# Performance work log

Hardware: AMD Instinct MI355X
Metric: run time of the kernel (lower is better)

Reference implementation:

```python
import jax, jax.numpy as jnp
import numpy as np

N = 100000
E = 1_600_000
D_IN, D_HID, D_OUT = 100, 512, 200
NUM_PATH_AGG = 5   # walks per node in sample_neighbors_and_aggregate
MAX_LEN = 4        # max walk length (incl. start node)
NUM_PATH_FINAL = 10  # global paths in sample_path


def _build_nbr(src, dst, n):
    """Padded neighbor table [n, max_deg] (int32) + degree vector [n]."""
    deg = np.zeros(n, np.int64)
    np.add.at(deg, src, 1)
    maxd = max(int(deg.max()), 1)
    nbr = np.zeros((n, maxd), np.int32)
    order = np.argsort(src, kind='stable')
    ssrc, sdst = src[order], dst[order]
    offs = np.zeros(n + 1, np.int64)
    offs[1:] = np.cumsum(deg)
    rank = np.arange(len(ssrc)) - offs[ssrc]
    nbr[ssrc, rank] = sdst
    return jnp.asarray(nbr), jnp.asarray(deg.astype(np.int32))


def setup_inputs() -> dict:
    key = jax.random.key(0)
    ks = jax.random.split(key, 4)
    x = jax.random.normal(ks[0], (N, D_IN), jnp.float32)
    edge_index = jax.random.randint(ks[1], (2, E), 0, N, jnp.int64)
    ei = np.asarray(edge_index)
    src, dst = ei[0], ei[1]
    # directed neighbor list (get_neighbor_list)
    nbr_dir, deg_dir = _build_nbr(src, dst, N)
    # bi-directional neighbor list (reverse edge added unless self-loop)
    m = src != dst
    nbr_bi, deg_bi = _build_nbr(np.concatenate([src, dst[m]]),
                                np.concatenate([dst, src[m]]), N)
    W1 = jax.random.normal(ks[2], (D_HID, D_IN), jnp.float32) * 0.05
    b1 = jnp.zeros((D_HID,), jnp.float32)
    W3 = jax.random.normal(ks[3], (D_OUT, D_HID), jnp.float32) * 0.05
    b3 = jnp.zeros((D_OUT,), jnp.float32)
    return dict(x=x, edge_index=edge_index, nbr_bi=nbr_bi, deg_bi=deg_bi,
                nbr_dir=nbr_dir, deg_dir=deg_dir, W1=W1, b1=b1, W3=W3, b3=b3)


def _random_walk(key, starts, nbr, deg, extra_steps):
    """Vectorized random walks. Returns nodes [L, M], masks [L, M] (bool).
    A step is invalid (walk stopped) once the current node has no neighbors."""
    cur = starts
    valid = jnp.ones(starts.shape, bool)
    nodes, masks = [cur], [valid]
    for j in range(extra_steps):
        u = jax.random.uniform(jax.random.fold_in(key, j), starts.shape)
        d = deg[cur]
        choice = jnp.minimum((u * d.astype(u.dtype)).astype(jnp.int32),
                             jnp.maximum(d - 1, 0))
        valid = valid & (d > 0)
        cur = jnp.where(valid, nbr[cur, choice], cur)
        nodes.append(cur)
        masks.append(valid)
    return jnp.stack(nodes), jnp.stack(masks)


def reference(x, edge_index, nbr_bi, deg_bi, nbr_dir, deg_dir, W1, b1, W3, b3):
    n = x.shape[0]
    kw = jax.random.key(42)
    # out = relu(fc1(x))
    h = jax.nn.relu(x @ W1.T + b1)  # [N, D_HID]

    # sample_neighbors_and_aggregate: 5 walks of length<=4 starting at every node
    starts1 = jnp.tile(jnp.arange(n, dtype=jnp.int32), NUM_PATH_AGG)  # [5N]
    nodes1, masks1 = _random_walk(jax.random.fold_in(kw, 0), starts1,
                                  nbr_bi, deg_bi, MAX_LEN - 1)
    # [L, 5N] -> [L*5, N]; tile concatenates copies so axis split is (L, 5, N)
    entries = nodes1.reshape(MAX_LEN, NUM_PATH_AGG, n).reshape(-1, n)
    mentries = masks1.reshape(MAX_LEN, NUM_PATH_AGG, n).reshape(-1, n)

    def body(carry, sm):
        acc, cnt = carry
        s, m = sm
        acc = acc + jnp.where(m[:, None], h[s], 0.0)  # masked gather [N, D_HID]
        cnt = cnt + m.astype(h.dtype)
        return (acc, cnt), None

    (acc, cnt), _ = jax.lax.scan(
        body, (jnp.zeros_like(h), jnp.zeros((n,), h.dtype)), (entries, mentries))
    agg = acc / cnt[:, None]  # per-node mean over visited nodes (cnt >= 5)

    # out = relu(fc3(agg))
    out2 = jax.nn.relu(agg @ W3.T + b3)  # [N, D_OUT]

    # sample_path: 10 walks from random start nodes on the DIRECTED graph
    starts2 = jax.random.randint(jax.random.fold_in(kw, 1),
                                 (NUM_PATH_FINAL,), 0, n, jnp.int32)
    nodes2, masks2 = _random_walk(jax.random.fold_in(kw, 2), starts2,
                                  nbr_dir, deg_dir, MAX_LEN - 1)
    g = out2[nodes2]                         # [L, 10, D_OUT]
    w = masks2.astype(out2.dtype)            # [L, 10]
    mean = (g * w[..., None]).sum((0, 1)) / w.sum()
    return mean[None, None, :]               # [1, 1, D_OUT] (matches torch keepdims)
```

## Files before the change

### kernel.cpp

```cpp
#include <hip/hip_runtime.h>
#include <stdint.h>
#include <string.h>

#define JAX_THREEFRY_PARTITIONABLE 1

#define DIN 100
#define DHID 512
#define DOUT 200
#define NPATH_AGG 5
#define NFINAL 10
#define MAXLEN 4
#define NSLOT (MAXLEN * NFINAL)
#define NE 16
#define QSPLIT 8
#define NBLK_P1 (NSLOT * QSPLIT)

struct RngConsts {
  uint32_t kA[3][2];
  int      starts2[NFINAL];
  float    u2[3][NFINAL];
  int      N, maxd_bi, maxd_dir;
};

__host__ __device__ inline void tf2x32(uint32_t k0, uint32_t k1,
                                       uint32_t& x0, uint32_t& x1) {
  const uint32_t k2 = k0 ^ k1 ^ 0x1BD11BDAu;
  x0 += k0; x1 += k1;
#define TFR(r) { x0 += x1; x1 = (x1 << (r)) | (x1 >> (32 - (r))); x1 ^= x0; }
  TFR(13) TFR(15) TFR(26) TFR(6)
  x0 += k1; x1 += k2 + 1u;
  TFR(17) TFR(29) TFR(16) TFR(24)
  x0 += k2; x1 += k0 + 2u;
  TFR(13) TFR(15) TFR(26) TFR(6)
  x0 += k0; x1 += k1 + 3u;
  TFR(17) TFR(29) TFR(16) TFR(24)
  x0 += k1; x1 += k2 + 4u;
  TFR(13) TFR(15) TFR(26) TFR(6)
  x0 += k2; x1 += k0 + 5u;
#undef TFR
}

__host__ __device__ inline uint32_t jax_bits32(uint32_t k0, uint32_t k1,
                                               uint32_t idx, uint32_t half) {
#if JAX_THREEFRY_PARTITIONABLE
  (void)half;
  uint32_t x0 = 0u, x1 = idx;
  tf2x32(k0, k1, x0, x1);
  return x0 ^ x1;
#else
  uint32_t x0, x1;
  const bool lo = idx < half;
  if (lo) { x0 = idx;        x1 = idx + half; }
  else    { x0 = idx - half; x1 = idx;        }
  tf2x32(k0, k1, x0, x1);
  return lo ? x0 : x1;
#endif
}

__host__ __device__ inline float bits_to_unif(uint32_t bits) {
  uint32_t f = (bits >> 9) | 0x3F800000u;
  float r;
  memcpy(&r, &f, 4);
  return r - 1.0f;
}

__device__ __forceinline__ void walk_step(const int* __restrict__ nbr,
                                          const int* __restrict__ deg,
                                          int maxd, int lane, float u,
                                          int& cur, int& valid) {
  const int d = deg[cur];
  const long long base = (long long)cur * maxd;
  int r0 = 0, r1 = 0, r2 = 0, r3 = 0;
  if (lane < maxd)       r0 = nbr[base + lane];
  if (lane + 64 < maxd)  r1 = nbr[base + lane + 64];
  if (lane + 128 < maxd) r2 = nbr[base + lane + 128];
  if (lane + 192 < maxd) r3 = nbr[base + lane + 192];
  int c = (int)(u * (float)d);
  const int cm = (d - 1 > 0) ? (d - 1) : 0;
  if (c > cm) c = cm;
  const int cl = c & 63;
  const int v0 = __shfl(r0, cl);
  const int v1 = __shfl(r1, cl);
  const int v2 = __shfl(r2, cl);
  const int v3 = __shfl(r3, cl);
  int v = (c < 64) ? v0 : (c < 128) ? v1 : (c < 192) ? v2 : v3;
  if (c >= 256) v = nbr[base + c];
  valid = valid && (d > 0);
  if (valid) cur = v;
}

__device__ __forceinline__ void stage_row(const float* __restrict__ x,
                                          float* __restrict__ dst,
                                          int node, int lane) {
  if (lane < DIN / 2) {
    *(float2*)(dst + lane * 2) =
        *(const float2*)(x + (long long)node * DIN + lane * 2);
  }
}

__global__ __launch_bounds__(512) void k_slot(
    const float* __restrict__ x,
    const int* __restrict__ nbr_bi, const int* __restrict__ deg_bi,
    const int* __restrict__ nbr_dir, const int* __restrict__ deg_dir,
    const float* __restrict__ W1, const float* __restrict__ b1,
    RngConsts rc, int* __restrict__ maskArr, float* __restrict__ aggAll) {
  __shared__ int   vmask[NE];
  __shared__ float xs[NE][DIN];

  const int bid = blockIdx.x;
  const int tid = threadIdx.x;
  const int wv = tid >> 6, lane = tid & 63;
  const int slot = bid >> 3, q = bid & (QSPLIT - 1);
  const int w = slot % NFINAL, j = slot / NFINAL;

  int cur = rc.starts2[w];
  int valid = 1;
  for (int t = 0; t < j; ++t)
    walk_step(nbr_dir, deg_dir, rc.maxd_dir, lane, rc.u2[t][w], cur, valid);

  if (q == 0 && tid == 0) maskArr[slot] = valid;
  if (!valid) return;

  const int n = cur;
  if (tid == 0) vmask[0] = 1;

  if (wv < NPATH_AGG) {
    const uint32_t wkr = (uint32_t)(wv * rc.N + n);
    int c2 = n, v2 = 1;
#pragma unroll
    for (int jj = 0; jj < MAXLEN - 1; ++jj) {
      const float u = bits_to_unif(
          jax_bits32(rc.kA[jj][0], rc.kA[jj][1], wkr, 250000u));
      walk_step(nbr_bi, deg_bi, rc.maxd_bi, lane, u, c2, v2);
      const int ent = 1 + jj * NPATH_AGG + wv;
      if (lane == 0) vmask[ent] = v2;
      stage_row(x, &xs[ent][0], c2, lane);
    }
  } else if (wv == 5) {
    stage_row(x, &xs[0][0], n, lane);
  }
  __syncthreads();

  const int usub = tid >> 3, ks = tid & 7;
  const int unit = q * 64 + usub;
  const float4* __restrict__ w1r = (const float4*)(W1 + (long long)unit * DIN);
  float acc[NE];
#pragma unroll
  for (int e = 0; e < NE; ++e) acc[e] = 0.0f;
  for (int k4 = ks; k4 < DIN / 4; k4 += 8) {
    const float4 wv4 = w1r[k4];
#pragma unroll
    for (int e = 0; e < NE; ++e) {
      const float4 xv = *(const float4*)(&xs[e][k4 * 4]);
      acc[e] += wv4.x * xv.x + wv4.y * xv.y + wv4.z * xv.z + wv4.w * xv.w;
    }
  }
#pragma unroll
  for (int e = 0; e < NE; ++e) {
    float p = acc[e];
    p += __shfl_xor(p, 1);
    p += __shfl_xor(p, 2);
    p += __shfl_xor(p, 4);
    acc[e] = p;
  }
  if (ks == 0) {
    float cntf = 5.0f;
#pragma unroll
    for (int e = 1; e < NE; ++e) cntf += (float)vmask[e];
    const float bb = b1[unit];
    float h0 = acc[0] + bb;
    h0 = (h0 > 0.0f) ? h0 : 0.0f;
    float hs = 5.0f * h0;
#pragma unroll
    for (int e = 1; e < NE; ++e) {
      if (vmask[e]) {
        const float hv = acc[e] + bb;
        hs += (hv > 0.0f) ? hv : 0.0f;
      }
    }
    aggAll[(long long)slot * DHID + unit] = hs / cntf;
  }
}

__global__ __launch_bounds__(512) void k_fc3(
    const float* __restrict__ W3, const float* __restrict__ b3,
    const int* __restrict__ maskArr, const float* __restrict__ aggAll,
    float* __restrict__ out) {
  __shared__ int   maskS[NSLOT];
  __shared__ float partial[8];

  const int o = blockIdx.x;
  const int tid = threadIdx.x;
  const int wv = tid >> 6, lane = tid & 63;

  if (tid < NSLOT) maskS[tid] = maskArr[tid];
  __syncthreads();

  const float4* __restrict__ w4 = (const float4*)(W3 + (long long)o * DHID);
  const float4 g0 = w4[lane];
  const float4 g1 = w4[64 + lane];
  const float b3o = b3[o];

  float acc = 0.0f;
#pragma unroll
  for (int i = 0; i < NSLOT / 8; ++i) {
    const int s = wv + i * 8;
    if (maskS[s]) {
      const float4* a4 = (const float4*)(aggAll + (long long)s * DHID);
      const float4 a0 = a4[lane];
      const float4 a1 = a4[64 + lane];
      float p = a0.x * g0.x + a0.y * g0.y + a0.z * g0.z + a0.w * g0.w
              + a1.x * g1.x + a1.y * g1.y + a1.z * g1.z + a1.w * g1.w;
#pragma unroll
      for (int off = 32; off; off >>= 1) p += __shfl_xor(p, off);
      const float r = p + b3o;
      acc += (r > 0.0f) ? r : 0.0f;
    }
  }
  if (lane == 0) partial[wv] = acc;
  __syncthreads();
  if (tid == 0) {
    float wsum = 0.0f;
    for (int s = 0; s < NSLOT; ++s) wsum += (float)maskS[s];
    float tot = 0.0f;
#pragma unroll
    for (int v = 0; v < 8; ++v) tot += partial[v];
    out[o] = tot / wsum;
  }
}

static void h_enc(const uint32_t k[2], uint32_t x0, uint32_t x1, uint32_t out[2]) {
  tf2x32(k[0], k[1], x0, x1);
  out[0] = x0; out[1] = x1;
}
static void h_foldin(const uint32_t k[2], uint32_t data, uint32_t out[2]) {
  h_enc(k, 0u, data, out);
}

extern "C" void kernel_launch(void* const* d_in, const int* in_sizes, int n_in,
                              void* d_out, int out_size, void* d_ws, size_t ws_size,
                              hipStream_t stream) {
  const float* x       = (const float*)d_in[0];
  const int*   nbr_bi  = (const int*)d_in[2];
  const int*   deg_bi  = (const int*)d_in[3];
  const int*   nbr_dir = (const int*)d_in[4];
  const int*   deg_dir = (const int*)d_in[5];
  const float* W1      = (const float*)d_in[6];
  const float* b1      = (const float*)d_in[7];
  const float* W3      = (const float*)d_in[8];
  const float* b3      = (const float*)d_in[9];

  const int N = in_sizes[0] / DIN;
  RngConsts rc;
  rc.N = N;
  rc.maxd_bi  = in_sizes[2] / N;
  rc.maxd_dir = in_sizes[4] / N;

  const uint32_t kw[2] = {0u, 42u};
  uint32_t kA[2];
  h_foldin(kw, 0u, kA);
  for (uint32_t j = 0; j < 3; ++j) h_foldin(kA, j, rc.kA[j]);

  uint32_t kS[2];
  h_foldin(kw, 1u, kS);
  uint32_t k1_[2], k2_[2];
#if JAX_THREEFRY_PARTITIONABLE
  h_enc(kS, 0u, 0u, k1_);
  h_enc(kS, 0u, 1u, k2_);
#else
  {
    uint32_t a[2], b[2];
    h_enc(kS, 0u, 2u, a);
    h_enc(kS, 1u, 3u, b);
    k1_[0] = a[0]; k1_[1] = b[0];
    k2_[0] = a[1]; k2_[1] = b[1];
  }
#endif
  {
    const uint32_t span = (uint32_t)N;
    uint32_t mult = 65536u % span;
    mult = (uint32_t)(mult * mult) % span;
    for (uint32_t i = 0; i < NFINAL; ++i) {
      const uint32_t hi = jax_bits32(k1_[0], k1_[1], i, NFINAL / 2);
      const uint32_t lo = jax_bits32(k2_[0], k2_[1], i, NFINAL / 2);
      uint32_t off = (hi % span) * mult + (lo % span);
      off %= span;
      rc.starts2[i] = (int)off;
    }
  }

  uint32_t kP[2];
  h_foldin(kw, 2u, kP);
  for (uint32_t j = 0; j < 3; ++j) {
    uint32_t kPj[2];
    h_foldin(kP, j, kPj);
    for (uint32_t i = 0; i < NFINAL; ++i)
      rc.u2[j][i] = bits_to_unif(jax_bits32(kPj[0], kPj[1], i, NFINAL / 2));
  }

  int*   maskArr = (int*)d_ws;
  float* aggAll  = (float*)(maskArr + NSLOT);

  k_slot<<<NBLK_P1, 512, 0, stream>>>(x, nbr_bi, deg_bi, nbr_dir, deg_dir,
                                      W1, b1, rc, maskArr, aggAll);
  k_fc3<<<DOUT, 512, 0, stream>>>(W3, b3, maskArr, aggAll, (float*)d_out);
}
```

Baseline: 19.80 us.

## Fuse slot and fc3 kernels via atomic counter with last-arriving blocks computing fc3

Merges the two launches into one kernel. Each block bumps a global atomic counter after its slot work. The last 50 blocks to arrive each take 4 output units: they preload W3 rows, spin until all 320 blocks have finished, then do the fc3/ReLU/mean reduction. This removes the second kernel launch and its launch gap, at the cost of an extra memset, a spin-wait on the slowest block, and reliance on all blocks being co-resident or finishing in order.

```diff
diff --git a/kernel.cpp b/kernel.cpp
--- a/kernel.cpp
+++ b/kernel.cpp
@@ -14,6 +14,8 @@
 #define NE 16
 #define QSPLIT 8
 #define NBLK_P1 (NSLOT * QSPLIT)
+#define NSPIN 50
+#define OPB 4
 
 struct RngConsts {
   uint32_t kA[3][2];
@@ -98,14 +100,19 @@
   }
 }
 
-__global__ __launch_bounds__(512) void k_slot(
+__global__ __launch_bounds__(512) void k_fused(
     const float* __restrict__ x,
     const int* __restrict__ nbr_bi, const int* __restrict__ deg_bi,
     const int* __restrict__ nbr_dir, const int* __restrict__ deg_dir,
     const float* __restrict__ W1, const float* __restrict__ b1,
-    RngConsts rc, int* __restrict__ maskArr, float* __restrict__ aggAll) {
+    const float* __restrict__ W3, const float* __restrict__ b3,
+    RngConsts rc, int* __restrict__ maskArr, float* __restrict__ aggAll,
+    int* __restrict__ counter, float* __restrict__ out) {
   __shared__ int   vmask[NE];
   __shared__ float xs[NE][DIN];
+  __shared__ int   oldS;
+  __shared__ int   maskS[NSLOT];
+  __shared__ float partial[8][OPB];
 
   const int bid = blockIdx.x;
   const int tid = threadIdx.x;
@@ -119,113 +126,141 @@
     walk_step(nbr_dir, deg_dir, rc.maxd_dir, lane, rc.u2[t][w], cur, valid);
 
   if (q == 0 && tid == 0) maskArr[slot] = valid;
-  if (!valid) return;
-
-  const int n = cur;
-  if (tid == 0) vmask[0] = 1;
-
-  if (wv < NPATH_AGG) {
-    const uint32_t wkr = (uint32_t)(wv * rc.N + n);
-    int c2 = n, v2 = 1;
-#pragma unroll
-    for (int jj = 0; jj < MAXLEN - 1; ++jj) {
-      const float u = bits_to_unif(
-          jax_bits32(rc.kA[jj][0], rc.kA[jj][1], wkr, 250000u));
-      walk_step(nbr_bi, deg_bi, rc.maxd_bi, lane, u, c2, v2);
-      const int ent = 1 + jj * NPATH_AGG + wv;
-      if (lane == 0) vmask[ent] = v2;
-      stage_row(x, &xs[ent][0], c2, lane);
-    }
-  } else if (wv == 5) {
-    stage_row(x, &xs[0][0], n, lane);
-  }
-  __syncthreads();
-
-  const int usub = tid >> 3, ks = tid & 7;
-  const int unit = q * 64 + usub;
-  const float4* __restrict__ w1r = (const float4*)(W1 + (long long)unit * DIN);
-  float acc[NE];
-#pragma unroll
-  for (int e = 0; e < NE; ++e) acc[e] = 0.0f;
-  for (int k4 = ks; k4 < DIN / 4; k4 += 8) {
-    const float4 wv4 = w1r[k4];
+
+  if (valid) {
+    const int n = cur;
+    if (tid == 0) vmask[0] = 1;
+
+    if (wv < NPATH_AGG) {
+      const uint32_t wkr = (uint32_t)(wv * rc.N + n);
+      int c2 = n, v2 = 1;
+#pragma unroll
+      for (int jj = 0; jj < MAXLEN - 1; ++jj) {
+        const float u = bits_to_unif(
+            jax_bits32(rc.kA[jj][0], rc.kA[jj][1], wkr, 250000u));
+        walk_step(nbr_bi, deg_bi, rc.maxd_bi, lane, u, c2, v2);
+        const int ent = 1 + jj * NPATH_AGG + wv;
+        if (lane == 0) vmask[ent] = v2;
+        stage_row(x, &xs[ent][0], c2, lane);
+      }
+    } else if (wv == 5) {
+      stage_row(x, &xs[0][0], n, lane);
+    }
+    __syncthreads();
+
+    const int usub = tid >> 3, ks = tid & 7;
+    const int unit = q * 64 + usub;
+    const float4* __restrict__ w1r =
+        (const float4*)(W1 + (long long)unit * DIN);
+    float acc[NE];
+#pragma unroll
+    for (int e = 0; e < NE; ++e) acc[e] = 0.0f;
+    for (int k4 = ks; k4 < DIN / 4; k4 += 8) {
+      const float4 wv4 = w1r[k4];
+#pragma unroll
+      for (int e = 0; e < NE; ++e) {
+        const float4 xv = *(const float4*)(&xs[e][k4 * 4]);
+        acc[e] += wv4.x * xv.x + wv4.y * xv.y + wv4.z * xv.z + wv4.w * xv.w;
+      }
+    }
 #pragma unroll
     for (int e = 0; e < NE; ++e) {
-      const float4 xv = *(const float4*)(&xs[e][k4 * 4]);
-      acc[e] += wv4.x * xv.x + wv4.y * xv.y + wv4.z * xv.z + wv4.w * xv.w;
-    }
-  }
-#pragma unroll
-  for (int e = 0; e < NE; ++e) {
-    float p = acc[e];
-    p += __shfl_xor(p, 1);
-    p += __shfl_xor(p, 2);
-    p += __shfl_xor(p, 4);
-    acc[e] = p;
-  }
-  if (ks == 0) {
-    float cntf = 5.0f;
-#pragma unroll
-    for (int e = 1; e < NE; ++e) cntf += (float)vmask[e];
-    const float bb = b1[unit];
-    float h0 = acc[0] + bb;
-    h0 = (h0 > 0.0f) ? h0 : 0.0f;
-    float hs = 5.0f * h0;
-#pragma unroll
-    for (int e = 1; e < NE; ++e) {
-      if (vmask[e]) {
-        const float hv = acc[e] + bb;
-        hs += (hv > 0.0f) ? hv : 0.0f;
+      float p = acc[e];
+      p += __shfl_xor(p, 1);
+      p += __shfl_xor(p, 2);
+      p += __shfl_xor(p, 4);
+      acc[e] = p;
+    }
+    if (ks == 0) {
+      float cntf = 5.0f;
+#pragma unroll
+      for (int e = 1; e < NE; ++e) cntf += (float)vmask[e];
+      const float bb = b1[unit];
+      float h0 = acc[0] + bb;
+      h0 = (h0 > 0.0f) ? h0 : 0.0f;
+      float hs = 5.0f * h0;
+#pragma unroll
+      for (int e = 1; e < NE; ++e) {
+        if (vmask[e]) {
+          const float hv = acc[e] + bb;
+          hs += (hv > 0.0f) ? hv : 0.0f;
+        }
       }
-    }
-    aggAll[(long long)slot * DHID + unit] = hs / cntf;
-  }
-}
-
-__global__ __launch_bounds__(512) void k_fc3(
-    const float* __restrict__ W3, const float* __restrict__ b3,
-    const int* __restrict__ maskArr, const float* __restrict__ aggAll,
-    float* __restrict__ out) {
-  __shared__ int   maskS[NSLOT];
-  __shared__ float partial[8];
-
-  const int o = blockIdx.x;
-  const int tid = threadIdx.x;
-  const int wv = tid >> 6, lane = tid & 63;
+      aggAll[(long long)slot * DHID + unit] = hs / cntf;
+    }
+  }
+
+  __syncthreads();
+  if (tid == 0)
+    oldS = __hip_atomic_fetch_add(counter, 1, __ATOMIC_ACQ_REL,
+                                  __HIP_MEMORY_SCOPE_AGENT);
+  __syncthreads();
+  const int old = oldS;
+  if (old < NBLK_P1 - NSPIN) return;
+
+  const int role = old - (NBLK_P1 - NSPIN);
+  const int ob = role * OPB;
+
+  float4 g[OPB][2];
+  float  b3v[OPB];
+#pragma unroll
+  for (int i = 0; i < OPB; ++i) {
+    const float4* w4 = (const float4*)(W3 + (long long)(ob + i) * DHID);
+    g[i][0] = w4[lane];
+    g[i][1] = w4[64 + lane];
+    b3v[i] = b3[ob + i];
+  }
+
+  if (tid == 0) {
+    while (__hip_atomic_load(counter, __ATOMIC_RELAXED,
+                             __HIP_MEMORY_SCOPE_AGENT) < NBLK_P1) {
+      __builtin_amdgcn_s_sleep(2);
+    }
+  }
+  __syncthreads();
+  (void)__hip_atomic_load(counter, __ATOMIC_ACQUIRE, __HIP_MEMORY_SCOPE_AGENT);
 
   if (tid < NSLOT) maskS[tid] = maskArr[tid];
   __syncthreads();
 
-  const float4* __restrict__ w4 = (const float4*)(W3 + (long long)o * DHID);
-  const float4 g0 = w4[lane];
-  const float4 g1 = w4[64 + lane];
-  const float b3o = b3[o];
-
-  float acc = 0.0f;
-#pragma unroll
-  for (int i = 0; i < NSLOT / 8; ++i) {
-    const int s = wv + i * 8;
+  float accv[OPB];
+#pragma unroll
+  for (int i = 0; i < OPB; ++i) accv[i] = 0.0f;
+#pragma unroll
+  for (int si = 0; si < NSLOT / 8; ++si) {
+    const int s = wv + si * 8;
     if (maskS[s]) {
       const float4* a4 = (const float4*)(aggAll + (long long)s * DHID);
       const float4 a0 = a4[lane];
       const float4 a1 = a4[64 + lane];
-      float p = a0.x * g0.x + a0.y * g0.y + a0.z * g0.z + a0.w * g0.w
-              + a1.x * g1.x + a1.y * g1.y + a1.z * g1.z + a1.w * g1.w;
-#pragma unroll
-      for (int off = 32; off; off >>= 1) p += __shfl_xor(p, off);
-      const float r = p + b3o;
-      acc += (r > 0.0f) ? r : 0.0f;
-    }
-  }
-  if (lane == 0) partial[wv] = acc;
+#pragma unroll
+      for (int i = 0; i < OPB; ++i) {
+        float p = a0.x * g[i][0].x + a0.y * g[i][0].y
+                + a0.z * g[i][0].z + a0.w * g[i][0].w
+                + a1.x * g[i][1].x + a1.y * g[i][1].y
+                + a1.z * g[i][1].z + a1.w * g[i][1].w;
+#pragma unroll
+        for (int off = 32; off; off >>= 1) p += __shfl_xor(p, off);
+        const float r = p + b3v[i];
+        accv[i] += (r > 0.0f) ? r : 0.0f;
+      }
+    }
+  }
+  if (lane == 0) {
+#pragma unroll
+    for (int i = 0; i < OPB; ++i) partial[wv][i] = accv[i];
+  }
   __syncthreads();
   if (tid == 0) {
     float wsum = 0.0f;
     for (int s = 0; s < NSLOT; ++s) wsum += (float)maskS[s];
-    float tot = 0.0f;
-#pragma unroll
-    for (int v = 0; v < 8; ++v) tot += partial[v];
-    out[o] = tot / wsum;
+#pragma unroll
+    for (int i = 0; i < OPB; ++i) {
+      float tot = 0.0f;
+#pragma unroll
+      for (int v = 0; v < 8; ++v) tot += partial[v][i];
+      out[ob + i] = tot / wsum;
+    }
   }
 }
 
@@ -300,8 +335,10 @@
 
   int*   maskArr = (int*)d_ws;
   float* aggAll  = (float*)(maskArr + NSLOT);
-
-  k_slot<<<NBLK_P1, 512, 0, stream>>>(x, nbr_bi, deg_bi, nbr_dir, deg_dir,
-                                      W1, b1, rc, maskArr, aggAll);
-  k_fc3<<<DOUT, 512, 0, stream>>>(W3, b3, maskArr, aggAll, (float*)d_out);
-}
+  int*   counter = (int*)(aggAll + NSLOT * DHID);
+
+  hipMemsetAsync(counter, 0, sizeof(int), stream);
+  k_fused<<<NBLK_P1, 512, 0, stream>>>(x, nbr_bi, deg_bi, nbr_dir, deg_dir,
+                                       W1, b1, W3, b3, rc, maskArr, aggAll,
+                                       counter, (float*)d_out);
+}
```

Result: slower. 33.45 us (+69.0%).

## Fuse fc3 partial dot products into slot kernel, add tiny finale reduction

Applied to the files above, without the earlier changes.

Each slot block now stages its 64-unit slice of the aggregated hidden vector in shared memory and computes partial fc3 dot products against W3 for all outputs. It writes per-(output, slot, q-split) partials instead of the full hidden vectors. A small 64-thread finale kernel sums the partials, applies bias, ReLU and the masked mean. This moves the W3 matvec work into the first kernel to shrink the second kernel's work, at the cost of a scalar, uncoalesced-ish per-lane W3 read with 200 shuffle reductions per block and an extra partial buffer.

```diff
diff --git a/kernel.cpp b/kernel.cpp
--- a/kernel.cpp
+++ b/kernel.cpp
@@ -103,9 +103,11 @@
     const int* __restrict__ nbr_bi, const int* __restrict__ deg_bi,
     const int* __restrict__ nbr_dir, const int* __restrict__ deg_dir,
     const float* __restrict__ W1, const float* __restrict__ b1,
-    RngConsts rc, int* __restrict__ maskArr, float* __restrict__ aggAll) {
+    const float* __restrict__ W3,
+    RngConsts rc, int* __restrict__ maskArr, float* __restrict__ dotAcc) {
   __shared__ int   vmask[NE];
   __shared__ float xs[NE][DIN];
+  __shared__ float agg64[64];
 
   const int bid = blockIdx.x;
   const int tid = threadIdx.x;
@@ -120,7 +122,6 @@
 
   if (q == 0 && tid == 0) maskArr[slot] = valid;
   if (!valid) return;
-
   const int n = cur;
   if (tid == 0) vmask[0] = 1;
 
@@ -178,55 +179,49 @@
         hs += (hv > 0.0f) ? hv : 0.0f;
       }
     }
-    aggAll[(long long)slot * DHID + unit] = hs / cntf;
-  }
-}
-
-__global__ __launch_bounds__(512) void k_fc3(
-    const float* __restrict__ W3, const float* __restrict__ b3,
-    const int* __restrict__ maskArr, const float* __restrict__ aggAll,
-    float* __restrict__ out) {
-  __shared__ int   maskS[NSLOT];
-  __shared__ float partial[8];
-
+    agg64[usub] = hs / cntf;
+  }
+  __syncthreads();
+
+  const float av = agg64[lane];
+  const long long colbase = (long long)q * 64 + lane;
+#pragma unroll 5
+  for (int i = 0; i < DOUT / 8; ++i) {
+    const int o = wv * (DOUT / 8) + i;
+    float p = W3[(long long)o * DHID + colbase] * av;
+#pragma unroll
+    for (int off = 32; off; off >>= 1) p += __shfl_xor(p, off);
+    if (lane == 0)
+      dotAcc[((long long)o * NSLOT + slot) * QSPLIT + q] = p;
+  }
+}
+
+__global__ __launch_bounds__(64) void k_finale(
+    const float* __restrict__ dotAcc, const int* __restrict__ maskArr,
+    const float* __restrict__ b3, float* __restrict__ out) {
   const int o = blockIdx.x;
-  const int tid = threadIdx.x;
-  const int wv = tid >> 6, lane = tid & 63;
-
-  if (tid < NSLOT) maskS[tid] = maskArr[tid];
-  __syncthreads();
-
-  const float4* __restrict__ w4 = (const float4*)(W3 + (long long)o * DHID);
-  const float4 g0 = w4[lane];
-  const float4 g1 = w4[64 + lane];
-  const float b3o = b3[o];
-
-  float acc = 0.0f;
-#pragma unroll
-  for (int i = 0; i < NSLOT / 8; ++i) {
-    const int s = wv + i * 8;
-    if (maskS[s]) {
-      const float4* a4 = (const float4*)(aggAll + (long long)s * DHID);
-      const float4 a0 = a4[lane];
-      const float4 a1 = a4[64 + lane];
-      float p = a0.x * g0.x + a0.y * g0.y + a0.z * g0.z + a0.w * g0.w
-              + a1.x * g1.x + a1.y * g1.y + a1.z * g1.z + a1.w * g1.w;
-#pragma unroll
-      for (int off = 32; off; off >>= 1) p += __shfl_xor(p, off);
-      const float r = p + b3o;
-      acc += (r > 0.0f) ? r : 0.0f;
-    }
-  }
-  if (lane == 0) partial[wv] = acc;
-  __syncthreads();
-  if (tid == 0) {
-    float wsum = 0.0f;
-    for (int s = 0; s < NSLOT; ++s) wsum += (float)maskS[s];
-    float tot = 0.0f;
-#pragma unroll
-    for (int v = 0; v < 8; ++v) tot += partial[v];
-    out[o] = tot / wsum;
-  }
+  const int lane = threadIdx.x;
+
+  float contrib = 0.0f, mk = 0.0f;
+  if (lane < NSLOT) {
+    if (maskArr[lane]) {
+      mk = 1.0f;
+      const float4* p4 =
+          (const float4*)(dotAcc + ((long long)o * NSLOT + lane) * QSPLIT);
+      const float4 d0 = p4[0];
+      const float4 d1 = p4[1];
+      const float dot = ((d0.x + d0.y) + (d0.z + d0.w))
+                      + ((d1.x + d1.y) + (d1.z + d1.w));
+      const float r = dot + b3[o];
+      contrib = (r > 0.0f) ? r : 0.0f;
+    }
+  }
+#pragma unroll
+  for (int off = 32; off; off >>= 1) {
+    contrib += __shfl_xor(contrib, off);
+    mk += __shfl_xor(mk, off);
+  }
+  if (lane == 0) out[o] = contrib / mk;
 }
 
 static void h_enc(const uint32_t k[2], uint32_t x0, uint32_t x1, uint32_t out[2]) {
@@ -299,9 +294,9 @@
   }
 
   int*   maskArr = (int*)d_ws;
-  float* aggAll  = (float*)(maskArr + NSLOT);
+  float* dotAcc  = (float*)(maskArr + NSLOT);
 
   k_slot<<<NBLK_P1, 512, 0, stream>>>(x, nbr_bi, deg_bi, nbr_dir, deg_dir,
-                                      W1, b1, rc, maskArr, aggAll);
-  k_fc3<<<DOUT, 512, 0, stream>>>(W3, b3, maskArr, aggAll, (float*)d_out);
-}
+                                      W1, b1, W3, rc, maskArr, dotAcc);
+  k_finale<<<DOUT, 64, 0, stream>>>(dotAcc, maskArr, b3, (float*)d_out);
+}
```

Measured after the change: 25.53 us. 1.29x slower.
